# Kernel optimization log

Hardware: AMD Instinct MI355X
Metric: run time of the kernel (lower is better)

## Reference

```python
import jax, jax.numpy as jnp
import numpy as np

B, C, H, W, N = 16, 81, 128, 128, 64


def setup_inputs() -> dict:
    key = jax.random.key(0)
    k1, k2, k3, k4, k5 = jax.random.split(key, 5)
    bbox_pred = jax.random.normal(k1, (B, 4, H, W), jnp.float32)
    class_pred = jax.random.normal(k2, (B, C, H, W), jnp.float32)
    # well-formed GT boxes in [0,1]: x1y1 + positive wh
    xy = jax.random.uniform(k3, (B, N, 2), jnp.float32)
    wh = jax.random.uniform(k4, (B, N, 2), jnp.float32) * 0.5 + 0.05
    boxes = jnp.concatenate([xy, xy + wh], axis=-1)  # [B,N,4]
    labels = jax.random.randint(k5, (B, N), 0, C).astype(jnp.int32)
    return {"bbox_pred": bbox_pred, "class_pred": class_pred,
            "boxes": boxes, "labels": labels}


def reference(bbox_pred, class_pred, boxes, labels):
    Bb, Cc, Hh, Ww = class_pred.shape
    A = Hh * Ww
    pb = bbox_pred.transpose(0, 2, 3, 1).reshape(Bb, A, 4)   # [B,A,4]
    pc = class_pred.transpose(0, 2, 3, 1).reshape(Bb, A, Cc)  # [B,A,C]

    # pairwise IoU [B,A,N] via broadcasting (pred [B,A,1,4] vs gt [B,1,N,4])
    p = pb[:, :, None, :]
    g = boxes[:, None, :, :]
    ix1 = jnp.maximum(p[..., 0], g[..., 0])
    iy1 = jnp.maximum(p[..., 1], g[..., 1])
    ix2 = jnp.minimum(p[..., 2], g[..., 2])
    iy2 = jnp.minimum(p[..., 3], g[..., 3])
    inter = jnp.clip(ix2 - ix1, 0) * jnp.clip(iy2 - iy1, 0)
    pa = (pb[..., 2] - pb[..., 0]) * (pb[..., 3] - pb[..., 1])      # [B,A]
    ga = (boxes[..., 2] - boxes[..., 0]) * (boxes[..., 3] - boxes[..., 1])  # [B,N]
    union = pa[:, :, None] + ga[:, None, :] - inter
    ious = inter / union

    max_ious = ious.max(axis=-1)            # [B,A]
    max_idx = jnp.argmax(ious, axis=-1)     # [B,A]
    pos = max_ious > 0.5                    # [B,A]
    posf = pos.astype(pc.dtype)
    npos = posf.sum(axis=-1)                # [B]
    denom = jnp.maximum(npos, 1.0)

    assigned_labels = jnp.take_along_axis(labels, max_idx, axis=1)          # [B,A]
    assigned_boxes = jnp.take_along_axis(boxes, max_idx[..., None], axis=1)  # [B,A,4]

    # cross-entropy per anchor (mean over positives)
    logp = jax.nn.log_softmax(pc, axis=-1)
    ce = -jnp.take_along_axis(logp, assigned_labels[..., None], axis=2)[..., 0]
    cls_loss = (ce * posf).sum(axis=-1) / denom

    # smooth-L1 (beta=1), mean over positive elements (npos*4)
    diff = pb - assigned_boxes
    ad = jnp.abs(diff)
    sl1 = jnp.where(ad < 1.0, 0.5 * diff * diff, ad - 0.5)
    reg_loss = (sl1 * posf[..., None]).sum(axis=(-1, -2)) / (denom * 4.0)

    # fallback when an image has zero positives: CE with all-zero labels
    zero_loss = -logp[..., 0].mean(axis=-1)

    per_img = jnp.where(npos > 0, cls_loss + reg_loss, zero_loss)
    return per_img.mean()
```

## Files before the change

### kernel.cpp

```cpp
#include <hip/hip_runtime.h>
#include <math.h>

#define Bc 16
#define Cc 81
#define AA 16384
#define Nn 64
#define TPB 256
#define ILP 2
#define APB (TPB * ILP)
#define BLOCKS_PER_IMG (AA / APB)
#define NBLOCKS (Bc * BLOCKS_PER_IMG)

__global__ __launch_bounds__(TPB) void det_loss_main(
    const float* __restrict__ bbox_pred,
    const float* __restrict__ class_pred,
    const float* __restrict__ boxes,
    const int* __restrict__ labels,
    float* __restrict__ ws_part)
{
    __shared__ float4 sbox[Nn];
    __shared__ float  sga[Nn];
    __shared__ int    slab[Nn];

    const int blk  = blockIdx.x;
    const int b    = blk / BLOCKS_PER_IMG;
    const int ablk = blk % BLOCKS_PER_IMG;
    const int t    = threadIdx.x;

    if (t < Nn) {
        float4 g = ((const float4*)boxes)[b * Nn + t];
        sbox[t] = g;
        sga[t]  = (g.z - g.x) * (g.w - g.y);
        slab[t] = labels[b * Nn + t];
    }
    __syncthreads();

    const int a0 = ablk * APB + 2 * t;

    const float* bp = bbox_pred + (size_t)b * 4 * AA + a0;
    const float2 X1 = *(const float2*)(bp + 0 * AA);
    const float2 Y1 = *(const float2*)(bp + 1 * AA);
    const float2 X2 = *(const float2*)(bp + 2 * AA);
    const float2 Y2 = *(const float2*)(bp + 3 * AA);
    const float pa_0 = (X2.x - X1.x) * (Y2.x - Y1.x);
    const float pa_1 = (X2.y - X1.y) * (Y2.y - Y1.y);

    float best0 = -INFINITY, best1 = -INFINITY;
    int   j0 = 0, j1 = 0;
#pragma unroll 4
    for (int j = 0; j < Nn; ++j) {
        const float4 g  = sbox[j];
        const float  ga = sga[j];
        {
            const float ix1 = fmaxf(X1.x, g.x);
            const float iy1 = fmaxf(Y1.x, g.y);
            const float ix2 = fminf(X2.x, g.z);
            const float iy2 = fminf(Y2.x, g.w);
            const float inter = fmaxf(ix2 - ix1, 0.0f) * fmaxf(iy2 - iy1, 0.0f);
            const float iou = inter * __builtin_amdgcn_rcpf(pa_0 + ga - inter);
            if (iou > best0) { best0 = iou; j0 = j; }
        }
        {
            const float ix1 = fmaxf(X1.y, g.x);
            const float iy1 = fmaxf(Y1.y, g.y);
            const float ix2 = fminf(X2.y, g.z);
            const float iy2 = fminf(Y2.y, g.w);
            const float inter = fmaxf(ix2 - ix1, 0.0f) * fmaxf(iy2 - iy1, 0.0f);
            const float iou = inter * __builtin_amdgcn_rcpf(pa_1 + ga - inter);
            if (iou > best1) { best1 = iou; j1 = j; }
        }
    }
    const float posf0 = (best0 > 0.5f) ? 1.0f : 0.0f;
    const float posf1 = (best1 > 0.5f) ? 1.0f : 0.0f;
    const int    lab0 = slab[j0];
    const int    lab1 = slab[j1];
    const float4 gb0  = sbox[j0];
    const float4 gb1  = sbox[j1];

    const float* cp = class_pred + (size_t)b * Cc * AA + a0;
    const float2 c0 = *(const float2*)cp;
    float sA0 = __expf(c0.x), sA1 = __expf(c0.y);
    float sB0 = 0.0f,          sB1 = 0.0f;
#pragma unroll 8
    for (int c = 1; c < Cc; ++c) {
        const float2 x = *(const float2*)(cp + (size_t)c * AA);
        if (c & 1) { sB0 += __expf(x.x); sB1 += __expf(x.y); }
        else       { sA0 += __expf(x.x); sA1 += __expf(x.y); }
    }
    const float lse0 = __logf(sA0 + sB0);
    const float lse1 = __logf(sA1 + sB1);

    const float xl0 = class_pred[((size_t)b * Cc + lab0) * AA + a0];
    const float xl1 = class_pred[((size_t)b * Cc + lab1) * AA + a0 + 1];

    const float ce    = (lse0 - xl0) * posf0 + (lse1 - xl1) * posf1;
    const float logp0 = (c0.x - lse0) + (c0.y - lse1);

    float sl = 0.0f;
    {
        const float d0 = X1.x - gb0.x, d1 = Y1.x - gb0.y, d2 = X2.x - gb0.z, d3 = Y2.x - gb0.w;
        float s0 = 0.0f;
        const float a_0 = fabsf(d0), a_1 = fabsf(d1), a_2 = fabsf(d2), a_3 = fabsf(d3);
        s0 += (a_0 < 1.0f) ? 0.5f * d0 * d0 : a_0 - 0.5f;
        s0 += (a_1 < 1.0f) ? 0.5f * d1 * d1 : a_1 - 0.5f;
        s0 += (a_2 < 1.0f) ? 0.5f * d2 * d2 : a_2 - 0.5f;
        s0 += (a_3 < 1.0f) ? 0.5f * d3 * d3 : a_3 - 0.5f;
        sl += s0 * posf0;
    }
    {
        const float d0 = X1.y - gb1.x, d1 = Y1.y - gb1.y, d2 = X2.y - gb1.z, d3 = Y2.y - gb1.w;
        float s1 = 0.0f;
        const float a_0 = fabsf(d0), a_1 = fabsf(d1), a_2 = fabsf(d2), a_3 = fabsf(d3);
        s1 += (a_0 < 1.0f) ? 0.5f * d0 * d0 : a_0 - 0.5f;
        s1 += (a_1 < 1.0f) ? 0.5f * d1 * d1 : a_1 - 0.5f;
        s1 += (a_2 < 1.0f) ? 0.5f * d2 * d2 : a_2 - 0.5f;
        s1 += (a_3 < 1.0f) ? 0.5f * d3 * d3 : a_3 - 0.5f;
        sl += s1 * posf1;
    }

    float v0 = posf0 + posf1, v1 = ce, v2 = sl, v3 = logp0;
#pragma unroll
    for (int o = 32; o > 0; o >>= 1) {
        v0 += __shfl_down(v0, o);
        v1 += __shfl_down(v1, o);
        v2 += __shfl_down(v2, o);
        v3 += __shfl_down(v3, o);
    }
    __shared__ float red[4][4];
    const int wave = t >> 6, lane = t & 63;
    if (lane == 0) {
        red[wave][0] = v0; red[wave][1] = v1; red[wave][2] = v2; red[wave][3] = v3;
    }
    __syncthreads();
    if (t == 0) {
        float* o = ws_part + (size_t)blk * 4;
        o[0] = red[0][0] + red[1][0] + red[2][0] + red[3][0];
        o[1] = red[0][1] + red[1][1] + red[2][1] + red[3][1];
        o[2] = red[0][2] + red[1][2] + red[2][2] + red[3][2];
        o[3] = red[0][3] + red[1][3] + red[2][3] + red[3][3];
    }
}

__global__ __launch_bounds__(64) void det_loss_final(
    const float* __restrict__ ws_part, float* __restrict__ out)
{
    const int lane = threadIdx.x;
    float per = 0.0f;
    if (lane < Bc) {
        float npos = 0.0f, ce = 0.0f, sl = 0.0f, lp0 = 0.0f;
        for (int i = 0; i < BLOCKS_PER_IMG; ++i) {
            const float* p = ws_part + (size_t)(lane * BLOCKS_PER_IMG + i) * 4;
            npos += p[0]; ce += p[1]; sl += p[2]; lp0 += p[3];
        }
        const float denom = fmaxf(npos, 1.0f);
        const float cls_reg = ce / denom + sl / (denom * 4.0f);
        const float zero_loss = -lp0 / (float)AA;
        per = (npos > 0.0f) ? cls_reg : zero_loss;
    }
#pragma unroll
    for (int o = 8; o > 0; o >>= 1) per += __shfl_down(per, o);
    if (lane == 0) out[0] = per * (1.0f / (float)Bc);
}

extern "C" void kernel_launch(void* const* d_in, const int* in_sizes, int n_in,
                              void* d_out, int out_size, void* d_ws, size_t ws_size,
                              hipStream_t stream) {
    const float* bbox_pred  = (const float*)d_in[0];
    const float* class_pred = (const float*)d_in[1];
    const float* boxes      = (const float*)d_in[2];
    const int*   labels     = (const int*)d_in[3];
    float* out = (float*)d_out;
    float* ws  = (float*)d_ws;

    det_loss_main<<<NBLOCKS, TPB, 0, stream>>>(bbox_pred, class_pred, boxes, labels, ws);
    det_loss_final<<<1, 64, 0, stream>>>(ws, out);
}
```

Measured before the change: 28.55 us.

## Prefetch class logits in double-buffered groups overlapping IoU loop; parallelize final reduction

Issues the first group of nine class-logit loads before the IoU matching loop so memory latency overlaps the compute. The logsumexp then streams over the 81 classes in nine groups of nine, prefetching the next group into an alternate register buffer. The label-logit gather is moved earlier. The final reduction now uses 256 threads with shuffle-xor reductions over float4 partials instead of 16 serial threads, at the cost of higher register pressure in the main kernel.

```diff
diff --git a/kernel.cpp b/kernel.cpp
--- a/kernel.cpp
+++ b/kernel.cpp
@@ -10,13 +10,15 @@
 #define APB (TPB * ILP)
 #define BLOCKS_PER_IMG (AA / APB)
 #define NBLOCKS (Bc * BLOCKS_PER_IMG)
+#define G 9
+#define NG 9
 
 __global__ __launch_bounds__(TPB) void det_loss_main(
     const float* __restrict__ bbox_pred,
     const float* __restrict__ class_pred,
     const float* __restrict__ boxes,
     const int* __restrict__ labels,
-    float* __restrict__ ws_part)
+    float4* __restrict__ ws_part)
 {
     __shared__ float4 sbox[Nn];
     __shared__ float  sga[Nn];
@@ -45,9 +47,14 @@
     const float pa_0 = (X2.x - X1.x) * (Y2.x - Y1.x);
     const float pa_1 = (X2.y - X1.y) * (Y2.y - Y1.y);
 
+    const float* cp = class_pred + (size_t)b * Cc * AA + a0;
+    float2 buf0[G], buf1[G];
+#pragma unroll
+    for (int k = 0; k < G; ++k) buf0[k] = *(const float2*)(cp + (size_t)k * AA);
+
     float best0 = -INFINITY, best1 = -INFINITY;
     int   j0 = 0, j1 = 0;
-#pragma unroll 4
+#pragma unroll 8
     for (int j = 0; j < Nn; ++j) {
         const float4 g  = sbox[j];
         const float  ga = sga[j];
@@ -77,30 +84,43 @@
     const float4 gb0  = sbox[j0];
     const float4 gb1  = sbox[j1];
 
-    const float* cp = class_pred + (size_t)b * Cc * AA + a0;
-    const float2 c0 = *(const float2*)cp;
-    float sA0 = __expf(c0.x), sA1 = __expf(c0.y);
-    float sB0 = 0.0f,          sB1 = 0.0f;
-#pragma unroll 8
-    for (int c = 1; c < Cc; ++c) {
-        const float2 x = *(const float2*)(cp + (size_t)c * AA);
-        if (c & 1) { sB0 += __expf(x.x); sB1 += __expf(x.y); }
-        else       { sA0 += __expf(x.x); sA1 += __expf(x.y); }
+    const float xl0 = class_pred[((size_t)b * Cc + lab0) * AA + a0];
+    const float xl1 = class_pred[((size_t)b * Cc + lab1) * AA + a0 + 1];
+
+    float sA0 = 0.0f, sA1 = 0.0f, sB0 = 0.0f, sB1 = 0.0f;
+    float x00 = 0.0f, x01 = 0.0f;
+#pragma unroll
+    for (int g = 0; g < NG; ++g) {
+        if (g + 1 < NG) {
+            if ((g & 1) == 0) {
+#pragma unroll
+                for (int k = 0; k < G; ++k)
+                    buf1[k] = *(const float2*)(cp + (size_t)((g + 1) * G + k) * AA);
+            } else {
+#pragma unroll
+                for (int k = 0; k < G; ++k)
+                    buf0[k] = *(const float2*)(cp + (size_t)((g + 1) * G + k) * AA);
+            }
+        }
+#pragma unroll
+        for (int k = 0; k < G; ++k) {
+            const float2 x = ((g & 1) == 0) ? buf0[k] : buf1[k];
+            if (g == 0 && k == 0) { x00 = x.x; x01 = x.y; }
+            if (k & 1) { sB0 += __expf(x.x); sB1 += __expf(x.y); }
+            else       { sA0 += __expf(x.x); sA1 += __expf(x.y); }
+        }
     }
     const float lse0 = __logf(sA0 + sB0);
     const float lse1 = __logf(sA1 + sB1);
 
-    const float xl0 = class_pred[((size_t)b * Cc + lab0) * AA + a0];
-    const float xl1 = class_pred[((size_t)b * Cc + lab1) * AA + a0 + 1];
-
     const float ce    = (lse0 - xl0) * posf0 + (lse1 - xl1) * posf1;
-    const float logp0 = (c0.x - lse0) + (c0.y - lse1);
+    const float logp0 = (x00 - lse0) + (x01 - lse1);
 
     float sl = 0.0f;
     {
         const float d0 = X1.x - gb0.x, d1 = Y1.x - gb0.y, d2 = X2.x - gb0.z, d3 = Y2.x - gb0.w;
+        const float a_0 = fabsf(d0), a_1 = fabsf(d1), a_2 = fabsf(d2), a_3 = fabsf(d3);
         float s0 = 0.0f;
-        const float a_0 = fabsf(d0), a_1 = fabsf(d1), a_2 = fabsf(d2), a_3 = fabsf(d3);
         s0 += (a_0 < 1.0f) ? 0.5f * d0 * d0 : a_0 - 0.5f;
         s0 += (a_1 < 1.0f) ? 0.5f * d1 * d1 : a_1 - 0.5f;
         s0 += (a_2 < 1.0f) ? 0.5f * d2 * d2 : a_2 - 0.5f;
@@ -109,8 +129,8 @@
     }
     {
         const float d0 = X1.y - gb1.x, d1 = Y1.y - gb1.y, d2 = X2.y - gb1.z, d3 = Y2.y - gb1.w;
+        const float a_0 = fabsf(d0), a_1 = fabsf(d1), a_2 = fabsf(d2), a_3 = fabsf(d3);
         float s1 = 0.0f;
-        const float a_0 = fabsf(d0), a_1 = fabsf(d1), a_2 = fabsf(d2), a_3 = fabsf(d3);
         s1 += (a_0 < 1.0f) ? 0.5f * d0 * d0 : a_0 - 0.5f;
         s1 += (a_1 < 1.0f) ? 0.5f * d1 * d1 : a_1 - 0.5f;
         s1 += (a_2 < 1.0f) ? 0.5f * d2 * d2 : a_2 - 0.5f;
@@ -126,40 +146,52 @@
         v2 += __shfl_down(v2, o);
         v3 += __shfl_down(v3, o);
     }
-    __shared__ float red[4][4];
+    __shared__ float4 red[4];
     const int wave = t >> 6, lane = t & 63;
-    if (lane == 0) {
-        red[wave][0] = v0; red[wave][1] = v1; red[wave][2] = v2; red[wave][3] = v3;
-    }
+    if (lane == 0) red[wave] = make_float4(v0, v1, v2, v3);
     __syncthreads();
     if (t == 0) {
-        float* o = ws_part + (size_t)blk * 4;
-        o[0] = red[0][0] + red[1][0] + red[2][0] + red[3][0];
-        o[1] = red[0][1] + red[1][1] + red[2][1] + red[3][1];
-        o[2] = red[0][2] + red[1][2] + red[2][2] + red[3][2];
-        o[3] = red[0][3] + red[1][3] + red[2][3] + red[3][3];
+        float4 r0 = red[0], r1 = red[1], r2 = red[2], r3 = red[3];
+        ws_part[blk] = make_float4(r0.x + r1.x + r2.x + r3.x,
+                                   r0.y + r1.y + r2.y + r3.y,
+                                   r0.z + r1.z + r2.z + r3.z,
+                                   r0.w + r1.w + r2.w + r3.w);
     }
 }
 
-__global__ __launch_bounds__(64) void det_loss_final(
-    const float* __restrict__ ws_part, float* __restrict__ out)
+__global__ __launch_bounds__(256) void det_loss_final(
+    const float4* __restrict__ ws_part, float* __restrict__ out)
 {
-    const int lane = threadIdx.x;
+    const int t = threadIdx.x;
+    float4 p0 = ws_part[t];
+    float4 p1 = ws_part[t + 256];
+#pragma unroll
+    for (int o = 1; o < 32; o <<= 1) {
+        p0.x += __shfl_xor(p0.x, o); p0.y += __shfl_xor(p0.y, o);
+        p0.z += __shfl_xor(p0.z, o); p0.w += __shfl_xor(p0.w, o);
+        p1.x += __shfl_xor(p1.x, o); p1.y += __shfl_xor(p1.y, o);
+        p1.z += __shfl_xor(p1.z, o); p1.w += __shfl_xor(p1.w, o);
+    }
+    __shared__ float4 simg[16];
+    const int lane = t & 63, w = t >> 6;
+    if (lane == 0 || lane == 32) {
+        const int img = 2 * w + (lane >> 5);
+        simg[img]     = p0;
+        simg[img + 8] = p1;
+    }
+    __syncthreads();
     float per = 0.0f;
-    if (lane < Bc) {
-        float npos = 0.0f, ce = 0.0f, sl = 0.0f, lp0 = 0.0f;
-        for (int i = 0; i < BLOCKS_PER_IMG; ++i) {
-            const float* p = ws_part + (size_t)(lane * BLOCKS_PER_IMG + i) * 4;
-            npos += p[0]; ce += p[1]; sl += p[2]; lp0 += p[3];
-        }
+    if (t < Bc) {
+        const float4 s = simg[t];
+        const float npos = s.x;
         const float denom = fmaxf(npos, 1.0f);
-        const float cls_reg = ce / denom + sl / (denom * 4.0f);
-        const float zero_loss = -lp0 / (float)AA;
+        const float cls_reg = s.y / denom + s.z / (denom * 4.0f);
+        const float zero_loss = -s.w / (float)AA;
         per = (npos > 0.0f) ? cls_reg : zero_loss;
     }
 #pragma unroll
     for (int o = 8; o > 0; o >>= 1) per += __shfl_down(per, o);
-    if (lane == 0) out[0] = per * (1.0f / (float)Bc);
+    if (t == 0) out[0] = per * (1.0f / (float)Bc);
 }
 
 extern "C" void kernel_launch(void* const* d_in, const int* in_sizes, int n_in,
@@ -170,8 +202,8 @@
     const float* boxes      = (const float*)d_in[2];
     const int*   labels     = (const int*)d_in[3];
     float* out = (float*)d_out;
-    float* ws  = (float*)d_ws;
+    float4* ws = (float4*)d_ws;
 
     det_loss_main<<<NBLOCKS, TPB, 0, stream>>>(bbox_pred, class_pred, boxes, labels, ws);
-    det_loss_final<<<1, 64, 0, stream>>>(ws, out);
+    det_loss_final<<<1, 256, 0, stream>>>(ws, out);
 }
```

New measurement: 25.14 us. -11.9%, faster.
